# Kernel optimization log

Hardware: AMD Instinct MI355X
Metric: run time of the kernel (lower is better)

Reference implementation:

```python
import jax, jax.numpy as jnp
import numpy as np

EMBED_DIM = 512
NUM_HEADS = 8
HEAD_DIM = EMBED_DIM // NUM_HEADS
B, N = 2, 4096


def setup_inputs() -> dict:
    key = jax.random.key(0)
    ks = jax.random.split(key, 5)
    x = jax.random.normal(ks[0], (B, N, EMBED_DIM), dtype=jnp.float32)
    # causal mask: 1 where attention is allowed (j <= i), 0 elsewhere
    mask = jnp.tril(jnp.ones((N, N), dtype=jnp.int32))[None, None]  # [1,1,N,N]
    s_in = 1.0 / np.sqrt(EMBED_DIM)
    qkv_w = jax.random.uniform(ks[1], (3 * EMBED_DIM, EMBED_DIM), jnp.float32, -s_in, s_in)
    qkv_b = jax.random.uniform(ks[2], (3 * EMBED_DIM,), jnp.float32, -s_in, s_in)
    out_w = jax.random.uniform(ks[3], (EMBED_DIM, EMBED_DIM), jnp.float32, -s_in, s_in)
    out_b = jax.random.uniform(ks[4], (EMBED_DIM,), jnp.float32, -s_in, s_in)
    return {"x": x, "mask": mask, "qkv_w": qkv_w, "qkv_b": qkv_b,
            "out_w": out_w, "out_b": out_b}


def reference(x, mask, qkv_w, qkv_b, out_w, out_b):
    Bc, Nc, C = x.shape
    H, D = NUM_HEADS, HEAD_DIM
    scale = D ** (-0.5)
    qkv = x @ qkv_w.T + qkv_b                      # [B,N,3C]
    qkv = qkv.reshape(Bc, Nc, 3, H, D)
    q = jnp.transpose(qkv[:, :, 0], (0, 2, 1, 3))  # [B,H,N,D]
    k = jnp.transpose(qkv[:, :, 1], (0, 2, 1, 3))
    v = jnp.transpose(qkv[:, :, 2], (0, 2, 1, 3))
    scores = jnp.einsum('bhqd,bhkd->bhqk', q, k) * scale
    scores = jnp.where(mask == 0, -jnp.inf, scores)
    attn = jax.nn.softmax(scores, axis=-1)         # dropout p=0 (eval)
    out = jnp.einsum('bhqk,bhkd->bhqd', attn, v)   # [B,H,N,D]
    out = jnp.transpose(out, (0, 2, 1, 3)).reshape(Bc, Nc, C)
    return out @ out_w.T + out_b
```

## Files before the change

### kernel.cpp

```cpp
#include <hip/hip_runtime.h>
#include <hip/hip_bf16.h>
#include <cstdint>
#include <cstddef>

#define EMBED 512
#define NHEADS 8
#define HDIM 64
#define BATCH 2
#define SEQ 4096
#define TOKENS (BATCH*SEQ)
#define QSCALE 0.1803368801f

typedef __attribute__((ext_vector_type(8))) short short8;
typedef __attribute__((ext_vector_type(4))) float floatx4;

#if defined(__has_builtin)
# if __has_builtin(__builtin_amdgcn_exp2f)
#  define EXP2F(x) __builtin_amdgcn_exp2f(x)
# else
#  define EXP2F(x) exp2f(x)
# endif
#else
# define EXP2F(x) exp2f(x)
#endif

union U8 { uint4 u; short8 s; };

__device__ __forceinline__ unsigned short f2bf(float f){
  unsigned int u = __float_as_uint(f);
  u += 0x7fff + ((u >> 16) & 1);
  return (unsigned short)(u >> 16);
}

__device__ __forceinline__ unsigned int pkbf(float a, float b){
  unsigned int ra = __float_as_uint(a) + 0x8000u;
  unsigned int rb = __float_as_uint(b) + 0x8000u;
  return __builtin_amdgcn_perm(rb, ra, 0x07060302u);
}

__device__ __forceinline__ void gl2lds16(const unsigned short* g, unsigned short* l){
  __builtin_amdgcn_global_load_lds(
      (const __attribute__((address_space(1))) unsigned int*)g,
      (__attribute__((address_space(3))) unsigned int*)l, 16, 0, 0);
}

#define XN4  (TOKENS*EMBED/4)
#define W1N4 (3*EMBED*EMBED/4)
#define W2N4 (EMBED*EMBED/4)
__global__ void cvt_all(const float* __restrict__ x, const float* __restrict__ w1,
                        const float* __restrict__ w2, unsigned short* __restrict__ out){
  int i = blockIdx.x*blockDim.x + threadIdx.x;
  const float* s; int j;
  if (i < XN4){ s = x; j = i; }
  else if (i < XN4+W1N4){ s = w1; j = i - XN4; }
  else { s = w2; j = i - (XN4+W1N4); }
  float4 v = reinterpret_cast<const float4*>(s)[j];
  ushort4 o; o.x=f2bf(v.x); o.y=f2bf(v.y); o.z=f2bf(v.z); o.w=f2bf(v.w);
  reinterpret_cast<ushort4*>(out)[i] = o;
}

template<int MODE>
__global__ __launch_bounds__(256) void gemm_bt(
    const unsigned short* __restrict__ A,
    const unsigned short* __restrict__ Bw,
    const float* __restrict__ bias,
    unsigned short* __restrict__ Qb,
    unsigned short* __restrict__ Kb,
    unsigned short* __restrict__ Vb,
    float* __restrict__ Cout)
{
  const int K = EMBED;
  __shared__ unsigned short Al[128*64];
  __shared__ unsigned short Bl[128*64];
  const int tm = blockIdx.x * 128;
  const int tn = blockIdx.y * 128;
  const int tid = threadIdx.x;
  const int w = tid >> 6, lane = tid & 63;
  const int m16 = lane & 15, q4 = lane >> 4;
  const int wm = w & 1, wn = w >> 1;
  const bool transp = (MODE == 1) || (tn < 2*EMBED);

  floatx4 acc[4][4];
  #pragma unroll
  for (int i=0;i<4;i++)
    #pragma unroll
    for (int j=0;j<4;j++) acc[i][j] = (floatx4){0.f,0.f,0.f,0.f};

  const int srow = tid >> 3, p8 = tid & 7, c8 = p8 ^ (srow & 7);

  for (int k0 = 0; k0 < K; k0 += 64){
    __syncthreads();
    #pragma unroll
    for (int cal=0; cal<4; cal++){
      gl2lds16(A  + (size_t)(tm + cal*32 + srow)*K + k0 + c8*8, Al + cal*2048 + tid*8);
      gl2lds16(Bw + (size_t)(tn + cal*32 + srow)*K + k0 + c8*8, Bl + cal*2048 + tid*8);
    }
    __syncthreads();
    short8 af[4][2], bfv[4][2];
    #pragma unroll
    for (int i=0;i<4;i++)
      #pragma unroll
      for (int s=0;s<2;s++)
        af[i][s] = *reinterpret_cast<const short8*>(Al + (wm*64 + i*16 + m16)*64 + (((s*4+q4) ^ (m16&7))*8));
    #pragma unroll
    for (int j=0;j<4;j++)
      #pragma unroll
      for (int s=0;s<2;s++)
        bfv[j][s] = *reinterpret_cast<const short8*>(Bl + (wn*64 + j*16 + m16)*64 + (((s*4+q4) ^ (m16&7))*8));
    #pragma unroll
    for (int i=0;i<4;i++)
      #pragma unroll
      for (int j=0;j<4;j++)
        #pragma unroll
        for (int s=0;s<2;s++){
          if (transp)
            acc[i][j] = __builtin_amdgcn_mfma_f32_16x16x32_bf16(bfv[j][s], af[i][s], acc[i][j], 0,0,0);
          else
            acc[i][j] = __builtin_amdgcn_mfma_f32_16x16x32_bf16(af[i][s], bfv[j][s], acc[i][j], 0,0,0);
        }
  }

  if (MODE == 1){
    #pragma unroll
    for (int j=0;j<4;j++){
      const int col0 = tn + wn*64 + j*16 + q4*4;
      const float4 bv = *reinterpret_cast<const float4*>(bias + col0);
      #pragma unroll
      for (int i=0;i<4;i++){
        const int row = tm + wm*64 + i*16 + m16;
        float4 o;
        o.x = acc[i][j][0] + bv.x; o.y = acc[i][j][1] + bv.y;
        o.z = acc[i][j][2] + bv.z; o.w = acc[i][j][3] + bv.w;
        *reinterpret_cast<float4*>(Cout + (size_t)row*EMBED + col0) = o;
      }
    }
    return;
  }

  if (transp){
    #pragma unroll
    for (int j=0;j<4;j++){
      const int col0 = tn + wn*64 + j*16 + q4*4;
      const int which = col0 >> 9, h = (col0 >> 6) & 7, d0 = col0 & 63;
      const float4 bv = *reinterpret_cast<const float4*>(bias + col0);
      #pragma unroll
      for (int i=0;i<4;i++){
        const int row = tm + wm*64 + i*16 + m16;
        const int b = row >> 12, n = row & (SEQ-1);
        float v0 = acc[i][j][0] + bv.x, v1 = acc[i][j][1] + bv.y;
        float v2 = acc[i][j][2] + bv.z, v3 = acc[i][j][3] + bv.w;
        unsigned short* dst;
        if (which == 0){
          v0 *= QSCALE; v1 *= QSCALE; v2 *= QSCALE; v3 *= QSCALE;
          dst = Qb + ((size_t)(b*NHEADS + h)*SEQ + n)*HDIM + d0;
        } else {
          dst = Kb + ((size_t)(b*NHEADS + h)*SEQ + n)*HDIM + d0;
        }
        uint2 pk; pk.x = pkbf(v0, v1); pk.y = pkbf(v2, v3);
        *reinterpret_cast<uint2*>(dst) = pk;
      }
    }
  } else {
    #pragma unroll
    for (int j=0;j<4;j++){
      const int col = tn + wn*64 + j*16 + m16;
      const float bv = bias[col];
      const int h = (col >> 6) & 7, d = col & 63;
      #pragma unroll
      for (int i=0;i<4;i++){
        const int row0 = tm + wm*64 + i*16 + q4*4;
        const int b = row0 >> 12, n0 = row0 & (SEQ-1);
        uint2 pk;
        pk.x = pkbf(acc[i][j][0] + bv, acc[i][j][1] + bv);
        pk.y = pkbf(acc[i][j][2] + bv, acc[i][j][3] + bv);
        *reinterpret_cast<uint2*>(Vb + ((size_t)(b*NHEADS + h)*HDIM + d)*SEQ + n0) = pk;
      }
    }
  }
}

__global__ __launch_bounds__(256, 4) void flash_attn(
  const unsigned short* __restrict__ Qb,
  const unsigned short* __restrict__ Kb,
  const unsigned short* __restrict__ Vb,
  unsigned short* __restrict__ Ob)
{
  __shared__ unsigned short KVl[2][2*64*64];

  const int blk = blockIdx.x;
  const int qt = (blk < 512) ? (63 - (blk >> 4)) : ((blk >> 4) - 32);
  const int bh = blk & 15;
  const int qbase = qt * 64;
  const unsigned short* Qh = Qb + (size_t)bh*SEQ*HDIM;
  const unsigned short* Kh = Kb + (size_t)bh*SEQ*HDIM;
  const unsigned short* Vh = Vb + (size_t)bh*HDIM*SEQ;

  const int tid = threadIdx.x, w = tid>>6, lane = tid&63;
  const int m16 = lane & 15, q4 = lane >> 4;
  const int srow = tid >> 3, p8 = tid & 7, c8 = p8 ^ (srow & 7);
  const int x7 = m16 & 7;
  const int q4l = q4 & 1, q4h = q4 >> 1;

  short8 ones;
  #pragma unroll
  for (int i=0;i<8;i++) ones[i] = (short)0x3F80;

  const int rowg0 = qbase + w*16;
  short8 qf0, qf1;
  {
    const unsigned short* qp = Qh + (size_t)(rowg0 + m16)*HDIM + q4*8;
    qf0 = *reinterpret_cast<const short8*>(qp);
    qf1 = *reinterpret_cast<const short8*>(qp + 32);
  }

  floatx4 oacc[4];
  floatx4 lacc = (floatx4){0.f,0.f,0.f,0.f};
  #pragma unroll
  for (int t=0;t<4;t++) oacc[t] = (floatx4){0.f,0.f,0.f,0.f};

  const unsigned short* ks = Kh + (size_t)srow*HDIM + c8*8;
  const unsigned short* vs = Vh + (size_t)srow*SEQ + c8*8;

  gl2lds16(ks,            &KVl[0][tid*8]);
  gl2lds16(ks + 32*HDIM,  &KVl[0][32*64 + tid*8]);
  gl2lds16(vs,            &KVl[0][64*64 + tid*8]);
  gl2lds16(vs + 32*SEQ,   &KVl[0][64*64 + 32*64 + tid*8]);
  ks += 64*HDIM; vs += 64;

  for (int jt = 0; jt <= qt; jt++){
    const int cur = jt & 1;
    const int jbase = jt*64;
    __syncthreads();
    if (jt < qt){
      unsigned short* dst = &KVl[cur^1][0];
      gl2lds16(ks,           dst + tid*8);
      gl2lds16(ks + 32*HDIM, dst + 32*64 + tid*8);
      gl2lds16(vs,           dst + 64*64 + tid*8);
      gl2lds16(vs + 32*SEQ,  dst + 64*64 + 32*64 + tid*8);
      ks += 64*HDIM; vs += 64;
    }
    if (jbase > rowg0 + 15) continue;
    const unsigned short* Kl = &KVl[cur][0];
    const unsigned short* Vl = &KVl[cur][64*64];

    floatx4 s[4];
    #pragma unroll
    for (int t=0;t<4;t++){
      floatx4 a = (floatx4){0.f,0.f,0.f,0.f};
      short8 kf0 = *reinterpret_cast<const short8*>(Kl + (t*16 + m16)*64 + ((q4     ^ x7)*8));
      short8 kf1 = *reinterpret_cast<const short8*>(Kl + (t*16 + m16)*64 + (((q4+4) ^ x7)*8));
      a = __builtin_amdgcn_mfma_f32_16x16x32_bf16(kf0, qf0, a, 0,0,0);
      a = __builtin_amdgcn_mfma_f32_16x16x32_bf16(kf1, qf1, a, 0,0,0);
      s[t] = a;
    }

    if (jbase + 63 > rowg0){
      #pragma unroll
      for (int t=0;t<4;t++)
        #pragma unroll
        for (int r=0;r<4;r++){
          float p = EXP2F(s[t][r]);
          const int key = jbase + t*16 + q4*4 + r;
          if (key > rowg0 + m16) p = 0.f;
          s[t][r] = p;
        }
    } else {
      #pragma unroll
      for (int t=0;t<4;t++)
        #pragma unroll
        for (int r=0;r<4;r++)
          s[t][r] = EXP2F(s[t][r]);
    }

    short8 pf[2];
    #pragma unroll
    for (int tp=0; tp<2; tp++){
      U8 a;
      a.u.x = pkbf(s[2*tp][0],   s[2*tp][1]);
      a.u.y = pkbf(s[2*tp][2],   s[2*tp][3]);
      a.u.z = pkbf(s[2*tp+1][0], s[2*tp+1][1]);
      a.u.w = pkbf(s[2*tp+1][2], s[2*tp+1][3]);
      pf[tp] = a.s;
    }

    lacc = __builtin_amdgcn_mfma_f32_16x16x32_bf16(pf[0], ones, lacc, 0,0,0);
    lacc = __builtin_amdgcn_mfma_f32_16x16x32_bf16(pf[1], ones, lacc, 0,0,0);

    #pragma unroll
    for (int dt=0; dt<4; dt++){
      const unsigned short* vrow = Vl + (dt*16 + m16)*64;
      #pragma unroll
      for (int tp=0; tp<2; tp++){
        const int g0 = 4*tp + q4h, g1 = 4*tp + 2 + q4h;
        uint2 lo = *reinterpret_cast<const uint2*>(vrow + ((g0 ^ x7)*8) + q4l*4);
        uint2 hi = *reinterpret_cast<const uint2*>(vrow + ((g1 ^ x7)*8) + q4l*4);
        U8 vf; vf.u.x = lo.x; vf.u.y = lo.y; vf.u.z = hi.x; vf.u.w = hi.y;
        oacc[dt] = __builtin_amdgcn_mfma_f32_16x16x32_bf16(pf[tp], vf.s, oacc[dt], 0,0,0);
      }
    }
  }

  const int b = bh >> 3, h = bh & 7;
  #pragma unroll
  for (int r=0;r<4;r++){
    const float inv = 1.0f / lacc[r];
    const int n = rowg0 + q4*4 + r;
    const size_t base = ((size_t)(b*SEQ + n))*EMBED + h*HDIM;
    #pragma unroll
    for (int t=0;t<4;t++)
      Ob[base + t*16 + m16] = f2bf(oacc[t][r] * inv);
  }
}

extern "C" void kernel_launch(void* const* d_in, const int* in_sizes, int n_in,
                              void* d_out, int out_size, void* d_ws, size_t ws_size,
                              hipStream_t stream){
  const float* x      = (const float*)d_in[0];
  const float* qkv_w  = (const float*)d_in[2];
  const float* qkv_b  = (const float*)d_in[3];
  const float* out_w  = (const float*)d_in[4];
  const float* out_b  = (const float*)d_in[5];
  float* out = (float*)d_out;

  unsigned short* ws = (unsigned short*)d_ws;
  unsigned short* xb  = ws;
  unsigned short* qwb = xb  + (size_t)TOKENS*EMBED;
  unsigned short* owb = qwb + (size_t)3*EMBED*EMBED;
  unsigned short* Qb  = owb + (size_t)EMBED*EMBED;
  unsigned short* Kb  = Qb  + (size_t)BATCH*NHEADS*SEQ*HDIM;
  unsigned short* Vb  = Kb  + (size_t)BATCH*NHEADS*SEQ*HDIM;
  unsigned short* Ob  = Vb  + (size_t)BATCH*NHEADS*SEQ*HDIM;

  cvt_all<<<dim3((XN4+W1N4+W2N4)/256), 256, 0, stream>>>(x, qkv_w, out_w, xb);
  gemm_bt<0><<<dim3(TOKENS/128, 3*EMBED/128), 256, 0, stream>>>(xb, qwb, qkv_b, Qb, Kb, Vb, nullptr);
  flash_attn<<<dim3(SEQ/64*16), 256, 0, stream>>>(Qb, Kb, Vb, Ob);
  gemm_bt<1><<<dim3(TOKENS/128, EMBED/128), 256, 0, stream>>>(Ob, owb, out_b, nullptr, nullptr, nullptr, out);
}
```

Measured before the change: 209.5 us.

## Double-buffer GEMM LDS tiles and permute K rows for vectorized V reads

The projection GEMM now keeps two LDS buffers and prefetches the next K-slice while the current one is consumed. This removes one barrier per iteration and overlaps global-to-LDS loads with MFMA work. In the attention kernel, K rows are loaded in a permuted order so that the P fragment's key ordering matches contiguous V columns. Each V operand then becomes a single 16-byte LDS read instead of two 8-byte reads, with the causal mask key index adjusted to match. Doubling the GEMM LDS footprint may reduce occupancy.

```diff
diff --git a/kernel.cpp b/kernel.cpp
--- a/kernel.cpp
+++ b/kernel.cpp
@@ -70,8 +70,8 @@
     float* __restrict__ Cout)
 {
   const int K = EMBED;
-  __shared__ unsigned short Al[128*64];
-  __shared__ unsigned short Bl[128*64];
+  __shared__ unsigned short Al[2][128*64];
+  __shared__ unsigned short Bl[2][128*64];
   const int tm = blockIdx.x * 128;
   const int tn = blockIdx.y * 128;
   const int tid = threadIdx.x;
@@ -88,25 +88,30 @@
 
   const int srow = tid >> 3, p8 = tid & 7, c8 = p8 ^ (srow & 7);
 
+  auto stage = [&](int k0, int buf){
+    #pragma unroll
+    for (int cal=0; cal<4; cal++){
+      gl2lds16(A  + (size_t)(tm + cal*32 + srow)*K + k0 + c8*8, &Al[buf][cal*2048 + tid*8]);
+      gl2lds16(Bw + (size_t)(tn + cal*32 + srow)*K + k0 + c8*8, &Bl[buf][cal*2048 + tid*8]);
+    }
+  };
+
+  stage(0, 0);
   for (int k0 = 0; k0 < K; k0 += 64){
+    const int cur = (k0 >> 6) & 1;
     __syncthreads();
-    #pragma unroll
-    for (int cal=0; cal<4; cal++){
-      gl2lds16(A  + (size_t)(tm + cal*32 + srow)*K + k0 + c8*8, Al + cal*2048 + tid*8);
-      gl2lds16(Bw + (size_t)(tn + cal*32 + srow)*K + k0 + c8*8, Bl + cal*2048 + tid*8);
-    }
-    __syncthreads();
+    if (k0 + 64 < K) stage(k0 + 64, cur^1);
     short8 af[4][2], bfv[4][2];
     #pragma unroll
     for (int i=0;i<4;i++)
       #pragma unroll
       for (int s=0;s<2;s++)
-        af[i][s] = *reinterpret_cast<const short8*>(Al + (wm*64 + i*16 + m16)*64 + (((s*4+q4) ^ (m16&7))*8));
+        af[i][s] = *reinterpret_cast<const short8*>(&Al[cur][(wm*64 + i*16 + m16)*64 + (((s*4+q4) ^ (m16&7))*8)]);
     #pragma unroll
     for (int j=0;j<4;j++)
       #pragma unroll
       for (int s=0;s<2;s++)
-        bfv[j][s] = *reinterpret_cast<const short8*>(Bl + (wn*64 + j*16 + m16)*64 + (((s*4+q4) ^ (m16&7))*8));
+        bfv[j][s] = *reinterpret_cast<const short8*>(&Bl[cur][(wn*64 + j*16 + m16)*64 + (((s*4+q4) ^ (m16&7))*8)]);
     #pragma unroll
     for (int i=0;i<4;i++)
       #pragma unroll
@@ -199,7 +204,7 @@
   const int m16 = lane & 15, q4 = lane >> 4;
   const int srow = tid >> 3, p8 = tid & 7, c8 = p8 ^ (srow & 7);
   const int x7 = m16 & 7;
-  const int q4l = q4 & 1, q4h = q4 >> 1;
+  const int kprow = 8*((srow>>2)&3) + 4*(srow>>4) + (srow&3);
 
   short8 ones;
   #pragma unroll
@@ -218,7 +223,7 @@
   #pragma unroll
   for (int t=0;t<4;t++) oacc[t] = (floatx4){0.f,0.f,0.f,0.f};
 
-  const unsigned short* ks = Kh + (size_t)srow*HDIM + c8*8;
+  const unsigned short* ks = Kh + (size_t)kprow*HDIM + c8*8;
   const unsigned short* vs = Vh + (size_t)srow*SEQ + c8*8;
 
   gl2lds16(ks,            &KVl[0][tid*8]);
@@ -227,6 +232,7 @@
   gl2lds16(vs + 32*SEQ,   &KVl[0][64*64 + 32*64 + tid*8]);
   ks += 64*HDIM; vs += 64;
 
+  const int key8 = 8*q4;
   for (int jt = 0; jt <= qt; jt++){
     const int cur = jt & 1;
     const int jbase = jt*64;
@@ -256,14 +262,16 @@
 
     if (jbase + 63 > rowg0){
       #pragma unroll
-      for (int t=0;t<4;t++)
+      for (int t=0;t<4;t++){
+        const int kb = ((t>>1)<<5) + ((t&1)<<2);
         #pragma unroll
         for (int r=0;r<4;r++){
           float p = EXP2F(s[t][r]);
-          const int key = jbase + t*16 + q4*4 + r;
+          const int key = jbase + kb + key8 + r;
           if (key > rowg0 + m16) p = 0.f;
           s[t][r] = p;
         }
+      }
     } else {
       #pragma unroll
       for (int t=0;t<4;t++)
@@ -291,11 +299,8 @@
       const unsigned short* vrow = Vl + (dt*16 + m16)*64;
       #pragma unroll
       for (int tp=0; tp<2; tp++){
-        const int g0 = 4*tp + q4h, g1 = 4*tp + 2 + q4h;
-        uint2 lo = *reinterpret_cast<const uint2*>(vrow + ((g0 ^ x7)*8) + q4l*4);
-        uint2 hi = *reinterpret_cast<const uint2*>(vrow + ((g1 ^ x7)*8) + q4l*4);
-        U8 vf; vf.u.x = lo.x; vf.u.y = lo.y; vf.u.z = hi.x; vf.u.w = hi.y;
-        oacc[dt] = __builtin_amdgcn_mfma_f32_16x16x32_bf16(pf[tp], vf.s, oacc[dt], 0,0,0);
+        short8 vf = *reinterpret_cast<const short8*>(vrow + (((4*tp + q4) ^ x7)*8));
+        oacc[dt] = __builtin_amdgcn_mfma_f32_16x16x32_bf16(pf[tp], vf, oacc[dt], 0,0,0);
       }
     }
   }
```

Measured after the change: 201.5 us, median of 2. -3.8%, faster.
